# Kernel optimization log

Hardware: AMD Instinct MI355X
Metric: run time of the kernel (lower is better)

The kernel has to match this reference:

```python
import jax, jax.numpy as jnp
import numpy as np

B, N, D_IN = 8, 1369, 768
S, D, ITERS = 7, 256, 3
RES, SIGMA = 37, 5.0
EPS = 1e-8


def _ln(x, g, b):
    m = jnp.mean(x, -1, keepdims=True)
    v = jnp.mean((x - m) ** 2, -1, keepdims=True)
    return (x - m) * jax.lax.rsqrt(v + 1e-5) * g + b


def _abs_grid():
    xs = jnp.linspace(-1.0, 1.0, RES)
    ys = jnp.linspace(-1.0, 1.0, RES)
    gx, gy = jnp.meshgrid(xs, ys, indexing='xy')
    return jnp.stack([gx.reshape(-1), gy.reshape(-1)], axis=-1)  # [N,2]


def setup_inputs() -> dict:
    key = jax.random.key(0)
    ks = jax.random.split(key, 40)
    i = iter(range(40))
    def w(shape, scale=0.02):
        return (jax.random.normal(ks[next(i)], shape, jnp.float32) * scale).astype(jnp.float32)
    def zeros(shape):
        return jnp.zeros(shape, jnp.float32)
    xav = float(np.sqrt(6.0 / (S + D)))
    inp = {
        'inputs': jax.random.normal(ks[next(i)], (B, N, D_IN), jnp.float32),
        'slots_init_p': jax.random.uniform(ks[next(i)], (1, S, D), jnp.float32, -xav, xav),
        'S_s0': w((1, S, 1, 2)),
        'S_p0': w((1, S, 1, 2)),
        'im_ln1_g': jnp.ones((D_IN,), jnp.float32), 'im_ln1_b': zeros((D_IN,)),
        'im_w1': w((D_IN, D_IN)), 'im_b1': zeros((D_IN,)),
        'im_w2': w((D_IN, D)), 'im_b2': zeros((D,)),
        'im_ln2_g': jnp.ones((D,), jnp.float32), 'im_ln2_b': zeros((D,)),
        'Wq': w((D, D)), 'Wk': w((D, D)), 'Wv': w((D, D)),
        'g_w': w((2, D)), 'g_b': zeros((D,)),
        'f_w1': w((D, D)), 'f_b1': zeros((D,)),
        'f_w2': w((D, D)), 'f_b2': zeros((D,)),
        'ln_g': jnp.ones((D,), jnp.float32), 'ln_b': zeros((D,)),
        'gru_wih': w((D, 3 * D)), 'gru_whh': w((D, 3 * D)),
        'gru_bih': zeros((3 * D,)), 'gru_bhh': zeros((3 * D,)),
        'mlp_ln_g': jnp.ones((D,), jnp.float32), 'mlp_ln_b': zeros((D,)),
        'mlp_w1': w((D, 4 * D)), 'mlp_b1': zeros((4 * D,)),
        'mlp_w2': w((4 * D, D)), 'mlp_b2': zeros((D,)),
        'fin_w': w((D, D)), 'fin_b': zeros((D,)),
    }
    return inp


def reference(inputs, slots_init_p, S_s0, S_p0,
              im_ln1_g, im_ln1_b, im_w1, im_b1, im_w2, im_b2, im_ln2_g, im_ln2_b,
              Wq, Wk, Wv, g_w, g_b, f_w1, f_b1, f_w2, f_b2,
              ln_g, ln_b, gru_wih, gru_whh, gru_bih, gru_bhh,
              mlp_ln_g, mlp_ln_b, mlp_w1, mlp_b1, mlp_w2, mlp_b2,
              fin_w, fin_b):
    abs_grid = _abs_grid()                    # [N,2], constant buffer
    ag = abs_grid[None, None]                 # [1,1,N,2]
    scale = D ** (-0.5)

    slots = jnp.broadcast_to(slots_init_p, (B, S, D))
    slots_init = slots

    # initial_mlp: LN -> Linear -> ReLU -> Linear -> LN (dropout-free eval path)
    x = _ln(inputs, im_ln1_g, im_ln1_b)
    x = jax.nn.relu(x @ im_w1 + im_b1)
    x = x @ im_w2 + im_b2
    x = _ln(x, im_ln2_g, im_ln2_b)            # [B,N,D]
    KX = x @ Wk                                # slot-independent part of K(inputs)
    VX = x @ Wv

    S_p = jnp.broadcast_to(S_p0, (B, S, 1, 2))
    S_s = jnp.broadcast_to(S_s0, (B, S, 1, 2))

    def f_mlp(z):
        return jax.nn.relu(z @ f_w1 + f_b1) @ f_w2 + f_b2

    attn = None
    slots_prev = slots
    for t in range(ITERS + 1):
        if t == ITERS - 1:  # query_opt straight-through trick
            slots = jax.lax.stop_gradient(slots) + slots_init - jax.lax.stop_gradient(slots_init)
        slots_prev = slots
        sn = _ln(slots, ln_g, ln_b)
        rel = (ag - S_p) / (S_s * SIGMA)      # [B,S,N,2]
        grel = rel @ g_w + g_b                # [B,S,N,D]
        k = f_mlp(KX[:, None] + grel)         # [B,S,N,D]
        v = f_mlp(VX[:, None] + grel)
        q = sn @ Wq                           # [B,S,D]
        dots = jnp.einsum('bsd,bsnd->bsn', q, k) * scale
        attn = jax.nn.softmax(dots, axis=1) + EPS   # softmax over slots
        attn = attn / jnp.sum(attn, -1, keepdims=True)
        updates = jnp.einsum('bsnd,bsn->bsd', v, attn)
        S_p = jnp.einsum('bsn,nd->bsd', attn, abs_grid)[:, :, None, :]
        S_s = jnp.sqrt(jnp.einsum('bsnd,bsn->bsd', (ag - S_p) ** 2, attn))[:, :, None, :]
        if t != ITERS:
            # GRUCell (torch gate order r,z,n)
            gi = updates @ gru_wih + gru_bih
            gh = slots_prev @ gru_whh + gru_bhh
            i_r, i_z, i_n = jnp.split(gi, 3, axis=-1)
            h_r, h_z, h_n = jnp.split(gh, 3, axis=-1)
            r = jax.nn.sigmoid(i_r + h_r)
            z = jax.nn.sigmoid(i_z + h_z)
            n = jnp.tanh(i_n + r * h_n)
            slots = (1.0 - z) * n + z * slots_prev
            # residual pre-norm MLP (dropout identity in eval)
            m = _ln(slots, mlp_ln_g, mlp_ln_b)
            m = jax.nn.relu(m @ mlp_w1 + mlp_b1) @ mlp_w2 + mlp_b2
            slots = slots + m
    out = slots_prev @ fin_w + fin_b
    return out, attn
```

## Files before the change

### kernel.cpp

```cpp
#include <hip/hip_runtime.h>

constexpr int CB   = 8;
constexpr int CN   = 1369;
constexpr int CDIN = 768;
constexpr int CS   = 7;
constexpr int CD   = 256;
constexpr int CITERS = 3;
constexpr int CRES = 37;
constexpr float CSIGMA = 5.0f;
constexpr int CBS = CB * CS;
constexpr int CBN = CB * CN;
constexpr int CKV = 2 * CD;
constexpr float LNEPS = 1e-5f;
constexpr float ATTN_EPS = 1e-8f;

typedef unsigned short u16;
typedef short bs8 __attribute__((ext_vector_type(8)));
typedef float f4 __attribute__((ext_vector_type(4)));

__device__ __forceinline__ float ag_x(int n) { return -1.f + (float)(n % CRES) * (2.f / 36.f); }
__device__ __forceinline__ float ag_y(int n) { return -1.f + (float)(n / CRES) * (2.f / 36.f); }

__device__ __forceinline__ u16 bf_rne(float f) {
    unsigned u = __float_as_uint(f);
    return (u16)((u + 0x7FFFu + ((u >> 16) & 1u)) >> 16);
}
__device__ __forceinline__ float bf_to_f(u16 h) { return __uint_as_float(((unsigned)h) << 16); }

__device__ __forceinline__ void split2b(float v, u16& h, u16& m) {
    h = bf_rne(v);
    m = bf_rne(v - bf_to_f(h));
}

__device__ __forceinline__ void async16(const u16* g, u16* l) {
    __builtin_amdgcn_global_load_lds(
        (const __attribute__((address_space(1))) unsigned int*)g,
        (__attribute__((address_space(3))) unsigned int*)l, 16, 0, 0);
}

__device__ __forceinline__ float block_reduce_sum(float v, float* sbuf) {
    #pragma unroll
    for (int off = 32; off > 0; off >>= 1) v += __shfl_down(v, off, 64);
    if ((threadIdx.x & 63) == 0) sbuf[threadIdx.x >> 6] = v;
    __syncthreads();
    if (threadIdx.x == 0) sbuf[0] = sbuf[0] + sbuf[1] + sbuf[2] + sbuf[3];
    __syncthreads();
    float r = sbuf[0];
    __syncthreads();
    return r;
}

__device__ __forceinline__ float block_reduce_sum128(float v, float* sbuf) {
    #pragma unroll
    for (int off = 32; off > 0; off >>= 1) v += __shfl_down(v, off, 64);
    if ((threadIdx.x & 63) == 0) sbuf[threadIdx.x >> 6] = v;
    __syncthreads();
    float r = sbuf[0] + sbuf[1];
    __syncthreads();
    return r;
}

__global__ __launch_bounds__(256) void ln_planes_kernel(const float* __restrict__ in,
        u16* __restrict__ Yh, u16* __restrict__ Ym,
        const float* __restrict__ g, const float* __restrict__ b, int d) {
    __shared__ float sbuf[8];
    int row = blockIdx.x, t = threadIdx.x;
    const float* x = in + (size_t)row * d;
    float v0 = x[t], v1 = 0.f, v2 = 0.f;
    if (d > 256) { v1 = x[t + 256]; v2 = x[t + 512]; }
    float mean = block_reduce_sum(v0 + v1 + v2, sbuf) / d;
    float d0 = v0 - mean, d1 = v1 - mean, d2 = v2 - mean;
    float pv = (d > 256) ? (d0 * d0 + d1 * d1 + d2 * d2) : (d0 * d0);
    float var = block_reduce_sum(pv, sbuf) / d;
    float rstd = rsqrtf(var + LNEPS);
    {
        float y = d0 * rstd * g[t] + b[t];
        u16 h, m; split2b(y, h, m);
        Yh[(size_t)row * d + t] = h; Ym[(size_t)row * d + t] = m;
    }
    if (d > 256) {
        float y1 = d1 * rstd * g[t + 256] + b[t + 256];
        u16 h, m; split2b(y1, h, m);
        Yh[(size_t)row * d + t + 256] = h; Ym[(size_t)row * d + t + 256] = m;
        float y2 = d2 * rstd * g[t + 512] + b[t + 512];
        split2b(y2, h, m);
        Yh[(size_t)row * d + t + 512] = h; Ym[(size_t)row * d + t + 512] = m;
    }
}

__global__ __launch_bounds__(256) void transpose_split2z_kernel(
        const float* __restrict__ W1, u16* __restrict__ T1h, u16* __restrict__ T1m,
        const float* __restrict__ W2, u16* __restrict__ T2h, u16* __restrict__ T2m) {
    __shared__ float tile[32][33];
    const float* W; u16 *Th, *Tm; int N;
    if (blockIdx.z == 0) { W = W1; Th = T1h; Tm = T1m; N = CDIN; }
    else                 { W = W2; Th = T2h; Tm = T2m; N = CD; if (blockIdx.x >= CD / 32) return; }
    int K = CDIN;
    int nb = blockIdx.x * 32, kb = blockIdx.y * 32;
    int tx = threadIdx.x & 31, ty = threadIdx.x >> 5;
    #pragma unroll
    for (int i = 0; i < 32; i += 8)
        tile[ty + i][tx] = W[(size_t)(kb + ty + i) * N + nb + tx];
    __syncthreads();
    #pragma unroll
    for (int i = 0; i < 32; i += 8) {
        float v = tile[tx][ty + i];
        u16 h, m; split2b(v, h, m);
        size_t idx = (size_t)(nb + ty + i) * K + kb + tx;
        Th[idx] = h; Tm[idx] = m;
    }
}

__global__ __launch_bounds__(256) void wprep_kernel(
        const float* __restrict__ Wk, const float* __restrict__ Wv,
        const float* __restrict__ Wq,
        const float* __restrict__ f_w1, const float* __restrict__ f_w2,
        u16* __restrict__ kvth, u16* __restrict__ kvtm, float* __restrict__ Pq,
        const float* __restrict__ wih, float* __restrict__ Pg,
        const float* __restrict__ g_w, const float* __restrict__ g_b,
        const float* __restrict__ f_b1,
        float* __restrict__ G2, float* __restrict__ gb1,
        const float* __restrict__ f_b2, const float* __restrict__ bih,
        float* __restrict__ bg, float* __restrict__ wqb) {
    __shared__ float arow[CD];
    int bid = blockIdx.x;
    int n = threadIdx.x;
    if (bid < 512) {
        const float* A = (bid < 256) ? Wk : Wv;
        int k = bid & 255;
        size_t poff = (bid < 256) ? 0 : (size_t)CD * CD;
        arow[n] = A[k * CD + n];
        __syncthreads();
        float acc = 0.f;
        for (int j = 0; j < CD; j++) acc += arow[j] * f_w1[(size_t)j * CD + n];
        u16 h, m; split2b(acc, h, m);
        kvth[poff + (size_t)n * CD + k] = h;
        kvtm[poff + (size_t)n * CD + k] = m;
    } else if (bid < 768) {
        int k = bid - 512;
        arow[n] = Wq[k * CD + n];
        __syncthreads();
        float acc = 0.f;
        for (int c = 0; c < CD; c++) acc += arow[c] * f_w2[(size_t)n * CD + c];
        Pq[(size_t)k * CD + n] = acc;
    } else if (bid < 1536) {
        int bid2 = bid - 768;
        int k = bid2 & 255;
        int ny = bid2 >> 8;
        arow[n] = f_w2[k * CD + n];
        __syncthreads();
        int nn = ny * 256 + n;
        float acc = 0.f;
        for (int j = 0; j < CD; j++) acc += arow[j] * wih[(size_t)j * (3 * CD) + nn];
        Pg[(size_t)k * (3 * CD) + nn] = acc;
    } else if (bid == 1536) {
        float a0 = 0.f, a1 = 0.f, ab = 0.f;
        for (int j = 0; j < CD; j++) {
            float w = f_w1[j * CD + n];
            a0 += g_w[j] * w;
            a1 += g_w[CD + j] * w;
            ab += g_b[j] * w;
        }
        G2[n] = a0; G2[CD + n] = a1; gb1[n] = ab + f_b1[n];
    } else if (bid <= 1539) {
        int nn = (bid - 1537) * 256 + n;
        float s = bih[nn];
        for (int c = 0; c < CD; c++) s += f_b2[c] * wih[(size_t)c * (3 * CD) + nn];
        bg[nn] = s;
    } else {
        float s = 0.f;
        for (int c = 0; c < CD; c++) s += Wq[n * CD + c] * f_b2[c];
        wqb[n] = s;
    }
}

template<int BN, int NBUF>
__global__ __launch_bounds__(256)
void hgemm2(const u16* __restrict__ Ah, const u16* __restrict__ Am,
            const u16* __restrict__ Bh, const u16* __restrict__ Bm,
            int M, int N, int K, const float* __restrict__ bias, int relu,
            float* __restrict__ Cf, u16* __restrict__ Ch, u16* __restrict__ Cm) {
    constexpr int BP = BN * 32;
    constexpr int SB = 4096 + 2 * BP;
    constexpr int NI = 2 + 2 * (BN / 64);
    constexpr int NF = BN / 32;
    constexpr int PP = BN / 64;
    __shared__ u16 smem[NBUF][SB];
    const int tid = threadIdx.x;

    int bx = blockIdx.x, by = blockIdx.y;
    {
        int gx = gridDim.x;
        int nwg = gx * gridDim.y;
        if (!(nwg & 7)) {
            int bid = by * gx + bx;
            int cpx = nwg >> 3;
            int s = (bid & 7) * cpx + (bid >> 3);
            bx = s % gx; by = s / gx;
        }
    }
    const int m0 = by * 64, n0 = bx * BN;
    const int w = tid >> 6, lane = tid & 63;
    const int wm = w & 1, wn = w >> 1;
    const int l15 = lane & 15, l4 = lane >> 4;

    const u16* srcp[NI];
    int dsto[NI];
    #pragma unroll
    for (int i = 0; i < NI; i++) {
        const u16* bp; int row, r, c;
        if (i < 2) {
            int qq = tid;
            r = qq >> 2;
            c = (qq & 3) ^ ((r ^ (r >> 2)) & 3);
            bp = (i == 0) ? Ah : Am;
            row = m0 + r; row = row < M ? row : M - 1;
            dsto[i] = i * 2048 + w * 512;
        } else {
            int ii = i - 2;
            int plane = ii / PP;
            int sub = ii % PP;
            int qq = sub * 256 + tid;
            r = qq >> 2;
            c = (qq & 3) ^ ((r ^ (r >> 2)) & 3);
            bp = plane ? Bm : Bh;
            row = n0 + r;
            dsto[i] = 4096 + plane * BP + sub * 2048 + w * 512;
        }
        srcp[i] = bp + (size_t)row * K + c * 8;
    }

    f4 acc[2][NF];
    #pragma unroll
    for (int i = 0; i < 2; i++)
        #pragma unroll
        for (int j = 0; j < NF; j++) acc[i][j] = (f4){0.f, 0.f, 0.f, 0.f};

    const int cx8 = (l4 ^ (l15 & 3) ^ ((l15 >> 2) & 3)) * 8;

    const int ns = K / 32;
    #pragma unroll
    for (int d = 0; d < NBUF - 1; d++)
        #pragma unroll
        for (int i = 0; i < NI; i++) async16(srcp[i] + d * 32, &smem[d][dsto[i]]);

    u16* c0 = &smem[0][0];
    u16* c1 = &smem[NBUF > 1 ? 1 : 0][0];
    u16* c2 = &smem[NBUF - 1][0];

    for (int k = 0; k < ns; k++) {
        if constexpr (NBUF == 3) {
            if (k + 2 < ns) {
                #pragma unroll
                for (int i = 0; i < NI; i++) async16(srcp[i] + (k + 2) * 32, c2 + dsto[i]);
                if constexpr (BN == 64) asm volatile("s_waitcnt vmcnt(8)" ::: "memory");
                else                     asm volatile("s_waitcnt vmcnt(12)" ::: "memory");
            } else if (k + 1 < ns) {
                if constexpr (BN == 64) asm volatile("s_waitcnt vmcnt(4)" ::: "memory");
                else                     asm volatile("s_waitcnt vmcnt(6)" ::: "memory");
            } else {
                asm volatile("s_waitcnt vmcnt(0)" ::: "memory");
            }
        } else {
            if (k + 1 < ns) {
                #pragma unroll
                for (int i = 0; i < NI; i++) async16(srcp[i] + (k + 1) * 32, c1 + dsto[i]);
                if constexpr (BN == 64) asm volatile("s_waitcnt vmcnt(4)" ::: "memory");
                else                     asm volatile("s_waitcnt vmcnt(6)" ::: "memory");
            } else {
                asm volatile("s_waitcnt vmcnt(0)" ::: "memory");
            }
        }
        __builtin_amdgcn_s_barrier();
        bs8 ah[2], am[2], bh[NF], bm[NF];
        #pragma unroll
        for (int f = 0; f < 2; f++) {
            int oa = (wm * 32 + f * 16 + l15) * 32 + cx8;
            ah[f] = *(const bs8*)(c0 + oa);
            am[f] = *(const bs8*)(c0 + 2048 + oa);
        }
        #pragma unroll
        for (int f = 0; f < NF; f++) {
            int ob = (wn * (NF * 16) + f * 16 + l15) * 32 + cx8;
            bh[f] = *(const bs8*)(c0 + 4096 + ob);
            bm[f] = *(const bs8*)(c0 + 4096 + BP + ob);
        }
        #pragma unroll
        for (int mf = 0; mf < 2; mf++)
            #pragma unroll
            for (int nf = 0; nf < NF; nf++) {
                acc[mf][nf] = __builtin_amdgcn_mfma_f32_16x16x32_bf16(am[mf], bh[nf], acc[mf][nf], 0, 0, 0);
                acc[mf][nf] = __builtin_amdgcn_mfma_f32_16x16x32_bf16(ah[mf], bm[nf], acc[mf][nf], 0, 0, 0);
                acc[mf][nf] = __builtin_amdgcn_mfma_f32_16x16x32_bf16(ah[mf], bh[nf], acc[mf][nf], 0, 0, 0);
            }
        asm volatile("" ::: "memory");
        __builtin_amdgcn_s_barrier();
        if constexpr (NBUF == 3) { u16* t_ = c0; c0 = c1; c1 = c2; c2 = t_; }
        else                     { u16* t_ = c0; c0 = c1; c1 = t_; }
    }

    #pragma unroll
    for (int mf = 0; mf < 2; mf++)
        #pragma unroll
        for (int i = 0; i < 4; i++) {
            int grow = m0 + wm * 32 + mf * 16 + l4 * 4 + i;
            if (grow < M) {
                #pragma unroll
                for (int nf = 0; nf < NF; nf++) {
                    int col = n0 + wn * (NF * 16) + nf * 16 + l15;
                    float v = acc[mf][nf][i] + (bias ? bias[col] : 0.f);
                    if (relu) v = fmaxf(v, 0.f);
                    if (Cf) Cf[(size_t)grow * N + col] = v;
                    else {
                        u16 h, m; split2b(v, h, m);
                        Ch[(size_t)grow * N + col] = h;
                        Cm[(size_t)grow * N + col] = m;
                    }
                }
            }
        }
}

__global__ __launch_bounds__(128) void rowgemm_kernel(const float* __restrict__ A,
        const float* __restrict__ W, const float* __restrict__ bias,
        float* __restrict__ C, int N, int K, int relu,
        const float* __restrict__ resid, const float* __restrict__ resb) {
    __shared__ float sA[1024];
    int r = blockIdx.x;
    int c = blockIdx.y * 128 + threadIdx.x;
    for (int i = threadIdx.x; i < K; i += 128) sA[i] = A[(size_t)r * K + i];
    __syncthreads();
    float a0 = 0.f, a1 = 0.f, a2 = 0.f, a3 = 0.f;
    #pragma unroll 4
    for (int k = 0; k < K; k += 4) {
        a0 += sA[k]     * W[(size_t)k * N + c];
        a1 += sA[k + 1] * W[(size_t)(k + 1) * N + c];
        a2 += sA[k + 2] * W[(size_t)(k + 2) * N + c];
        a3 += sA[k + 3] * W[(size_t)(k + 3) * N + c];
    }
    float v = (a0 + a1) + (a2 + a3) + (bias ? bias[c] : 0.f);
    if (relu) v = fmaxf(v, 0.f);
    if (resid) v += resid[(size_t)r * N + c] + resb[c];
    C[(size_t)r * N + c] = v;
}

__global__ __launch_bounds__(128) void rowgemmG_kernel(
        const float* __restrict__ A0, const float* __restrict__ W0,
        const float* __restrict__ b0, float* __restrict__ C0,
        const float* __restrict__ A1, const float* __restrict__ W1,
        const float* __restrict__ b1, float* __restrict__ C1,
        const float* __restrict__ msum, int N, int K) {
    __shared__ float sA[256];
    const float* A = blockIdx.z ? A1 : A0;
    const float* W = blockIdx.z ? W1 : W0;
    const float* B = blockIdx.z ? b1 : b0;
    float* C = blockIdx.z ? C1 : C0;
    int r = blockIdx.x;
    int c = blockIdx.y * 128 + threadIdx.x;
    float scl = blockIdx.z ? 1.f : 1.f / msum[r * 8];
    for (int i = threadIdx.x; i < K; i += 128) sA[i] = A[(size_t)r * K + i] * scl;
    __syncthreads();
    float a0 = 0.f, a1 = 0.f, a2 = 0.f, a3 = 0.f;
    #pragma unroll 4
    for (int k = 0; k < K; k += 4) {
        a0 += sA[k]     * W[(size_t)k * N + c];
        a1 += sA[k + 1] * W[(size_t)(k + 1) * N + c];
        a2 += sA[k + 2] * W[(size_t)(k + 2) * N + c];
        a3 += sA[k + 3] * W[(size_t)(k + 3) * N + c];
    }
    C[(size_t)r * N + c] = (a0 + a1) + (a2 + a3) + B[c];
}

__global__ __launch_bounds__(256) void init_kernel(const float* __restrict__ slots_init_p,
        const float* __restrict__ S_s0, const float* __restrict__ S_p0,
        float* __restrict__ slots, float* __restrict__ S_s, float* __restrict__ S_p) {
    int bs = blockIdx.x, t = threadIdx.x;
    int s = bs % CS;
    slots[bs * CD + t] = slots_init_p[s * CD + t];
    if (t < 2) { S_s[bs * 2 + t] = S_s0[s * 2 + t]; S_p[bs * 2 + t] = S_p0[s * 2 + t]; }
}

__global__ __launch_bounds__(256) void ln_slots_q_kernel(const float* __restrict__ slots,
        const float* __restrict__ ln_g, const float* __restrict__ ln_b,
        const float* __restrict__ wqb, const float* __restrict__ Pq,
        float* __restrict__ qwb, float* __restrict__ qb0) {
    __shared__ float sbuf[8];
    __shared__ float sN[CD];
    int row = blockIdx.x, t = threadIdx.x;
    float x = slots[row * CD + t];
    float mean = block_reduce_sum(x, sbuf) / CD;
    float d0 = x - mean;
    float var = block_reduce_sum(d0 * d0, sbuf) / CD;
    float sn = d0 * rsqrtf(var + LNEPS) * ln_g[t] + ln_b[t];
    sN[t] = sn;
    float qb = block_reduce_sum(sn * wqb[t], sbuf);
    if (t == 0) qb0[row] = qb;
    __syncthreads();
    float acc = 0.f;
    #pragma unroll 4
    for (int k = 0; k < CD; k++) acc += sN[k] * Pq[(size_t)k * CD + t];
    qwb[row * CD + t] = acc;
}

__global__ __launch_bounds__(256) void slotsup_kernel(const float* __restrict__ h1b,
        const float* __restrict__ w2, const float* __restrict__ b2,
        const float* __restrict__ snewb,
        const float* __restrict__ ln_g, const float* __restrict__ ln_b,
        const float* __restrict__ wqb, const float* __restrict__ Pq,
        float* __restrict__ slots, float* __restrict__ qwb, float* __restrict__ qb0) {
    __shared__ float sbuf[8];
    __shared__ float sH[4 * CD];
    __shared__ float sN[CD];
    int row = blockIdx.x, t = threadIdx.x;
    for (int i = t; i < 4 * CD; i += 256) sH[i] = h1b[(size_t)row * 4 * CD + i];
    __syncthreads();
    float a0 = 0.f, a1 = 0.f, a2 = 0.f, a3 = 0.f;
    #pragma unroll 4
    for (int k = 0; k < 4 * CD; k += 4) {
        a0 += sH[k]     * w2[(size_t)k * CD + t];
        a1 += sH[k + 1] * w2[(size_t)(k + 1) * CD + t];
        a2 += sH[k + 2] * w2[(size_t)(k + 2) * CD + t];
        a3 += sH[k + 3] * w2[(size_t)(k + 3) * CD + t];
    }
    float v = (a0 + a1) + (a2 + a3) + 0.f;
    v += snewb[row * CD + t] + b2[t];
    slots[row * CD + t] = v;
    float mean = block_reduce_sum(v, sbuf) / CD;
    float d0 = v - mean;
    float var = block_reduce_sum(d0 * d0, sbuf) / CD;
    float sn = d0 * rsqrtf(var + LNEPS) * ln_g[t] + ln_b[t];
    sN[t] = sn;
    float qb = block_reduce_sum(sn * wqb[t], sbuf);
    if (t == 0) qb0[row] = qb;
    __syncthreads();
    float acc = 0.f;
    #pragma unroll 4
    for (int k = 0; k < CD; k++) acc += sN[k] * Pq[(size_t)k * CD + t];
    qwb[row * CD + t] = acc;
}

__global__ __launch_bounds__(256) void dotsv_kernel(const float* __restrict__ KVX,
        const float* __restrict__ S_p, const float* __restrict__ S_s,
        const float* __restrict__ msum_in, int useMsum,
        const float* __restrict__ G2, const float* __restrict__ gb1,
        const float* __restrict__ qw, const float* __restrict__ qb0,
        float* __restrict__ attn, float* __restrict__ Wacc,
        float* __restrict__ msum_out) {
    __shared__ float sred[4 * CD];
    int b = blockIdx.x;
    int w = threadIdx.x >> 6, l = threadIdx.x & 63;
    int k4 = l * 4;
    float4 g0 = *(const float4*)(G2 + k4);
    float4 g1 = *(const float4*)(G2 + CD + k4);
    float4 gb = *(const float4*)(gb1 + k4);
    float4 qwv[CS]; float px[CS], py[CS], ix[CS], iy[CS], q0[CS];
    #pragma unroll
    for (int s = 0; s < CS; s++) {
        int bs = b * CS + s;
        qwv[s] = *(const float4*)(qw + bs * CD + k4);
        if (useMsum) {
            const float* mp = msum_in + bs * 8;
            float m0 = mp[0];
            float pxv = mp[1] / m0, pyv = mp[2] / m0;
            float sx = sqrtf(fmaxf(mp[3] / m0 - pxv * pxv, 0.f));
            float sy = sqrtf(fmaxf(mp[4] / m0 - pyv * pyv, 0.f));
            px[s] = pxv; py[s] = pyv;
            ix[s] = 1.f / (sx * CSIGMA); iy[s] = 1.f / (sy * CSIGMA);
        } else {
            px[s] = S_p[2 * bs]; py[s] = S_p[2 * bs + 1];
            ix[s] = 1.f / (S_s[2 * bs] * CSIGMA); iy[s] = 1.f / (S_s[2 * bs + 1] * CSIGMA);
        }
        q0[s] = qb0[bs];
    }
    float4 acc[CS];
    #pragma unroll
    for (int s = 0; s < CS; s++) acc[s] = make_float4(0.f, 0.f, 0.f, 0.f);
    float wmv = 0.f;
    int sidx = l / 5;
    int jidx = l - sidx * 5;
    int nbase = blockIdx.y * 16 + w * 4;
    #pragma unroll
    for (int i = 0; i < 4; i++) {
        int n = nbase + i;
        int nc = n < CN ? n : CN - 1;
        const float* rowp = KVX + (size_t)(b * CN + nc) * CKV;
        float4 kx = *(const float4*)(rowp + k4);
        float ax = ag_x(nc), ay = ag_y(nc);
        float dsv[CS];
        #pragma unroll
        for (int s = 0; s < CS; s++) {
            float r0 = (ax - px[s]) * ix[s];
            float r1 = (ay - py[s]) * iy[s];
            float v0 = fmaxf(kx.x + r0 * g0.x + r1 * g1.x + gb.x, 0.f);
            float v1 = fmaxf(kx.y + r0 * g0.y + r1 * g1.y + gb.y, 0.f);
            float v2 = fmaxf(kx.z + r0 * g0.z + r1 * g1.z + gb.z, 0.f);
            float v3 = fmaxf(kx.w + r0 * g0.w + r1 * g1.w + gb.w, 0.f);
            float d = v0 * qwv[s].x + v1 * qwv[s].y + v2 * qwv[s].z + v3 * qwv[s].w;
            #pragma unroll
            for (int off = 32; off > 0; off >>= 1) d += __shfl_xor(d, off, 64);
            dsv[s] = 0.0625f * (d + q0[s]);
        }
        float mx = -1e30f;
        #pragma unroll
        for (int s = 0; s < CS; s++) mx = fmaxf(mx, dsv[s]);
        float sum = 0.f;
        #pragma unroll
        for (int s = 0; s < CS; s++) { dsv[s] = __expf(dsv[s] - mx); sum += dsv[s]; }
        float inv = 1.f / sum;
        #pragma unroll
        for (int s = 0; s < CS; s++) dsv[s] = dsv[s] * inv + ATTN_EPS;
        if (attn && l == 0 && n < CN) {
            #pragma unroll
            for (int s = 0; s < CS; s++)
                attn[(size_t)(b * CS + s) * CN + n] = dsv[s];
        }
        if (msum_out && n < CN) {
            float ax2 = ax * ax, ay2 = ay * ay;
            float a = dsv[0];
            a = (sidx == 1) ? dsv[1] : a;
            a = (sidx == 2) ? dsv[2] : a;
            a = (sidx == 3) ? dsv[3] : a;
            a = (sidx == 4) ? dsv[4] : a;
            a = (sidx == 5) ? dsv[5] : a;
            a = (sidx == 6) ? dsv[6] : a;
            float coef = 1.f;
            coef = (jidx == 1) ? ax : coef;
            coef = (jidx == 2) ? ay : coef;
            coef = (jidx == 3) ? ax2 : coef;
            coef = (jidx == 4) ? ay2 : coef;
            wmv += a * coef;
        }
        if (Wacc && n < CN) {
            float4 vx = *(const float4*)(rowp + CD + k4);
            #pragma unroll
            for (int s = 0; s < CS; s++) {
                float r0 = (ax - px[s]) * ix[s];
                float r1 = (ay - py[s]) * iy[s];
                float a = dsv[s];
                acc[s].x += a * fmaxf(vx.x + r0 * g0.x + r1 * g1.x + gb.x, 0.f);
                acc[s].y += a * fmaxf(vx.y + r0 * g0.y + r1 * g1.y + gb.y, 0.f);
                acc[s].z += a * fmaxf(vx.z + r0 * g0.z + r1 * g1.z + gb.z, 0.f);
                acc[s].w += a * fmaxf(vx.w + r0 * g0.w + r1 * g1.w + gb.w, 0.f);
            }
        }
    }
    if (Wacc) {
        for (int s = 0; s < CS; s++) {
            ((float4*)sred)[w * 64 + l] = acc[s];
            __syncthreads();
            if (threadIdx.x < CD) {
                float v = sred[threadIdx.x] + sred[CD + threadIdx.x]
                        + sred[2 * CD + threadIdx.x] + sred[3 * CD + threadIdx.x];
                atomicAdd(&Wacc[(size_t)(b * CS + s) * CD + threadIdx.x], v);
            }
            __syncthreads();
        }
    }
    if (msum_out) {
        if (l < 35) sred[w * 35 + l] = wmv;
        __syncthreads();
        if (threadIdx.x < 35) {
            float v = sred[threadIdx.x] + sred[35 + threadIdx.x]
                    + sred[70 + threadIdx.x] + sred[105 + threadIdx.x];
            int s = threadIdx.x / 5, j = threadIdx.x % 5;
            atomicAdd(&msum_out[(size_t)(b * CS + s) * 8 + j], v);
        }
    }
}

__global__ __launch_bounds__(256) void attn_scale_kernel(float* __restrict__ u,
        const float* __restrict__ msum) {
    int bs = blockIdx.x;
    float inv = 1.f / msum[(size_t)bs * 8];
    float* up = u + (size_t)bs * CN;
    for (int n = threadIdx.x; n < CN; n += 256) up[n] *= inv;
}

__global__ __launch_bounds__(128) void gate_mlp1_kernel(const float* __restrict__ giRaw,
        const float* __restrict__ ghRaw, const float* __restrict__ slots,
        const float* __restrict__ mg, const float* __restrict__ mb,
        const float* __restrict__ mlp_w1, const float* __restrict__ mlp_b1,
        float* __restrict__ snewb, float* __restrict__ h1b,
        float* __restrict__ WaccZ, float* __restrict__ msumZ) {
    __shared__ float sbuf[4];
    __shared__ float sM[CD];
    int row = blockIdx.x, t = threadIdx.x;
    float snew[2];
    #pragma unroll
    for (int e = 0; e < 2; e++) {
        int tt = t + e * 128;
        float gi0 = giRaw[row * 3 * CD + tt];
        float gi1 = giRaw[row * 3 * CD + CD + tt];
        float gi2 = giRaw[row * 3 * CD + 2 * CD + tt];
        float gh0 = ghRaw[row * 3 * CD + tt];
        float gh1 = ghRaw[row * 3 * CD + CD + tt];
        float gh2 = ghRaw[row * 3 * CD + 2 * CD + tt];
        float r = 1.f / (1.f + expf(-(gi0 + gh0)));
        float z = 1.f / (1.f + expf(-(gi1 + gh1)));
        float nn = tanhf(gi2 + r * gh2);
        snew[e] = (1.f - z) * nn + z * slots[row * CD + tt];
    }
    if (blockIdx.y == 0) {
        snewb[row * CD + t] = snew[0];
        snewb[row * CD + t + 128] = snew[1];
        WaccZ[row * CD + t] = 0.f;
        WaccZ[row * CD + t + 128] = 0.f;
        if (t < 8) msumZ[row * 8 + t] = 0.f;
    }
    float mean = block_reduce_sum128(snew[0] + snew[1], sbuf) / CD;
    float d0 = snew[0] - mean, d1 = snew[1] - mean;
    float var = block_reduce_sum128(d0 * d0 + d1 * d1, sbuf) / CD;
    float rstd = rsqrtf(var + LNEPS);
    sM[t]       = d0 * rstd * mg[t] + mb[t];
    sM[t + 128] = d1 * rstd * mg[t + 128] + mb[t + 128];
    __syncthreads();
    int c = blockIdx.y * 128 + t;
    float a0 = 0.f, a1 = 0.f, a2 = 0.f, a3 = 0.f;
    #pragma unroll 4
    for (int k = 0; k < CD; k += 4) {
        a0 += sM[k]     * mlp_w1[(size_t)k * (4 * CD) + c];
        a1 += sM[k + 1] * mlp_w1[(size_t)(k + 1) * (4 * CD) + c];
        a2 += sM[k + 2] * mlp_w1[(size_t)(k + 2) * (4 * CD) + c];
        a3 += sM[k + 3] * mlp_w1[(size_t)(k + 3) * (4 * CD) + c];
    }
    h1b[(size_t)row * (4 * CD) + c] = fmaxf((a0 + a1) + (a2 + a3) + mlp_b1[c], 0.f);
}

extern "C" void kernel_launch(void* const* d_in, const int* in_sizes, int n_in,
                              void* d_out, int out_size, void* d_ws, size_t ws_size,
                              hipStream_t stream) {
    (void)in_sizes; (void)n_in; (void)out_size;
    const float* inputs       = (const float*)d_in[0];
    const float* slots_init_p = (const float*)d_in[1];
    const float* S_s0         = (const float*)d_in[2];
    const float* S_p0         = (const float*)d_in[3];
    const float* im_ln1_g = (const float*)d_in[4];
    const float* im_ln1_b = (const float*)d_in[5];
    const float* im_w1    = (const float*)d_in[6];
    const float* im_b1    = (const float*)d_in[7];
    const float* im_w2    = (const float*)d_in[8];
    const float* im_b2    = (const float*)d_in[9];
    const float* im_ln2_g = (const float*)d_in[10];
    const float* im_ln2_b = (const float*)d_in[11];
    const float* Wq  = (const float*)d_in[12];
    const float* Wk  = (const float*)d_in[13];
    const float* Wv  = (const float*)d_in[14];
    const float* g_w = (const float*)d_in[15];
    const float* g_b = (const float*)d_in[16];
    const float* f_w1 = (const float*)d_in[17];
    const float* f_b1 = (const float*)d_in[18];
    const float* f_w2 = (const float*)d_in[19];
    const float* f_b2 = (const float*)d_in[20];
    const float* ln_g = (const float*)d_in[21];
    const float* ln_b = (const float*)d_in[22];
    const float* gru_wih = (const float*)d_in[23];
    const float* gru_whh = (const float*)d_in[24];
    const float* gru_bih = (const float*)d_in[25];
    const float* gru_bhh = (const float*)d_in[26];
    const float* mlp_ln_g = (const float*)d_in[27];
    const float* mlp_ln_b = (const float*)d_in[28];
    const float* mlp_w1 = (const float*)d_in[29];
    const float* mlp_b1 = (const float*)d_in[30];
    const float* mlp_w2 = (const float*)d_in[31];
    const float* mlp_b2 = (const float*)d_in[32];
    const float* fin_w = (const float*)d_in[33];
    const float* fin_b = (const float*)d_in[34];

    char* base = (char*)d_ws;
    size_t off = 0;
    auto take = [&](size_t bytes) { void* p = base + off; off += (bytes + 255) & ~(size_t)255; return p; };

    float* R1 = (float*)take((size_t)CBN * CDIN * 4);
    float* R2 = (float*)take((size_t)CBN * CDIN * 4);
    u16* w1th = (u16*)take((size_t)CDIN * CDIN * 2);
    u16* w1tm = (u16*)take((size_t)CDIN * CDIN * 2);
    u16* w2th = (u16*)take((size_t)CDIN * CD * 2);
    u16* w2tm = (u16*)take((size_t)CDIN * CD * 2);
    u16* kvth = (u16*)take((size_t)CKV * CD * 2);
    u16* kvtm = (u16*)take((size_t)CKV * CD * 2);
    float* G2b  = (float*)take((size_t)2 * CD * 4);
    float* gb1b = (float*)take((size_t)CD * 4);
    float* Pq   = (float*)take((size_t)CD * CD * 4);
    float* Pg   = (float*)take((size_t)CD * 3 * CD * 4);
    float* bgv  = (float*)take((size_t)3 * CD * 4);
    float* wqbb = (float*)take((size_t)CD * 4);
    float* qwb   = (float*)take((size_t)CBS * CD * 4);
    float* qb0b  = (float*)take((size_t)CBS * 4);
    float* Wacc  = (float*)take(((size_t)CBS * CD + 2 * CBS * 8) * 4);
    float* msumA = Wacc + (size_t)CBS * CD;
    float* msumB = msumA + (size_t)CBS * 8;
    float* giRaw = (float*)take((size_t)CBS * 3 * CD * 4);
    float* ghRaw = (float*)take((size_t)CBS * 3 * CD * 4);
    float* snewb = (float*)take((size_t)CBS * CD * 4);
    float* h1b   = (float*)take((size_t)CBS * 4 * CD * 4);
    float* S_pB  = (float*)take((size_t)CBS * 2 * 4);
    float* S_sB  = (float*)take((size_t)CBS * 2 * 4);
    float* slots = (float*)take((size_t)CBS * CD * 4);
    if (ws_size < off) return;

    float* msum[2] = {msumA, msumB};

    u16* xlnh = (u16*)R1;
    u16* xlnm = xlnh + (size_t)CBN * CDIN;
    u16* X1h  = (u16*)R2;
    u16* X1m  = X1h + (size_t)CBN * CDIN;
    float* xD = R1;
    u16* xDnh = (u16*)(R1 + (size_t)CBN * CD);
    u16* xDnm = xDnh + (size_t)CBN * CD;
    float* KVX = R2;

    float* out0 = (float*)d_out;
    float* attnb = out0 + CBS * CD;

    dim3 blk(256);
    const int gM = (CBN + 63) / 64;
    dim3 gridBN(CB, 86);

    transpose_split2z_kernel<<<dim3(CDIN/32, CDIN/32, 2), blk, 0, stream>>>(
        im_w1, w1th, w1tm, im_w2, w2th, w2tm);
    wprep_kernel<<<dim3(1541), blk, 0, stream>>>(Wk, Wv, Wq, f_w1, f_w2,
        kvth, kvtm, Pq, gru_wih, Pg, g_w, g_b, f_b1, G2b, gb1b,
        f_b2, gru_bih, bgv, wqbb);
    hipMemsetAsync(Wacc, 0, ((size_t)CBS * CD + 2 * CBS * 8) * sizeof(float), stream);

    ln_planes_kernel<<<CBN, blk, 0, stream>>>(inputs, xlnh, xlnm, im_ln1_g, im_ln1_b, CDIN);
    hgemm2<128,2><<<dim3(CDIN/128, gM), blk, 0, stream>>>(xlnh, xlnm, w1th, w1tm,
        CBN, CDIN, CDIN, im_b1, 1, nullptr, X1h, X1m);
    hgemm2<64,3><<<dim3(CD/64, gM), blk, 0, stream>>>(X1h, X1m, w2th, w2tm,
        CBN, CD, CDIN, im_b2, 0, xD, nullptr, nullptr);
    ln_planes_kernel<<<CBN, blk, 0, stream>>>(xD, xDnh, xDnm, im_ln2_g, im_ln2_b, CD);
    hgemm2<64,3><<<dim3(CKV/64, gM), blk, 0, stream>>>(xDnh, xDnm, kvth, kvtm,
        CBN, CKV, CD, nullptr, 0, KVX, nullptr, nullptr);
    init_kernel<<<CBS, blk, 0, stream>>>(slots_init_p, S_s0, S_p0, slots, S_sB, S_pB);

    ln_slots_q_kernel<<<CBS, blk, 0, stream>>>(slots, ln_g, ln_b, wqbb, Pq, qwb, qb0b);

    for (int t = 0; t < CITERS; t++) {
        dotsv_kernel<<<gridBN, blk, 0, stream>>>(KVX, S_pB, S_sB,
            msum[(t + 1) & 1], t > 0 ? 1 : 0, G2b, gb1b,
            qwb, qb0b, nullptr, Wacc, msum[t & 1]);
        rowgemmG_kernel<<<dim3(CBS, 3*CD/128, 2), dim3(128), 0, stream>>>(
            Wacc, Pg, bgv, giRaw, slots, gru_whh, gru_bhh, ghRaw, msum[t & 1], 3 * CD, CD);
        gate_mlp1_kernel<<<dim3(CBS, 8), dim3(128), 0, stream>>>(giRaw, ghRaw, slots,
            mlp_ln_g, mlp_ln_b, mlp_w1, mlp_b1, snewb, h1b, Wacc, msum[(t + 1) & 1]);
        slotsup_kernel<<<CBS, blk, 0, stream>>>(h1b, mlp_w2, mlp_b2, snewb,
            ln_g, ln_b, wqbb, Pq, slots, qwb, qb0b);
    }
    dotsv_kernel<<<gridBN, blk, 0, stream>>>(KVX, S_pB, S_sB,
        msum[0], 1, G2b, gb1b, qwb, qb0b, attnb, nullptr, msum[1]);
    attn_scale_kernel<<<CBS, blk, 0, stream>>>(attnb, msum[1]);

    rowgemm_kernel<<<dim3(CBS, CD/128), dim3(128), 0, stream>>>(slots, fin_w, fin_b,
        out0, CD, CD, 0, nullptr, nullptr);
}
```

Before: 613.8 us.

## Fuse MLP second layer into gate kernel via atomics and merge small launches

Moves the MLP w2 product into gate_mlp1_kernel: each block computes its 128-wide slice of the hidden layer, multiplies it by the matching rows of w2, and atomically accumulates into a slots accumulator. slotsup then reads and zeroes that accumulator instead of doing the full 1024-deep matvec. The init and slot-LN/q kernels are merged into one, and the attention rescale is merged with the final projection into a single launch. This is meant to cut kernel launches and the h1b round trip through global memory. In exchange it adds atomic contention and makes the floating-point summation order nondeterministic.

```diff
diff --git a/kernel.cpp b/kernel.cpp
--- a/kernel.cpp
+++ b/kernel.cpp
@@ -321,29 +321,6 @@
         }
 }
 
-__global__ __launch_bounds__(128) void rowgemm_kernel(const float* __restrict__ A,
-        const float* __restrict__ W, const float* __restrict__ bias,
-        float* __restrict__ C, int N, int K, int relu,
-        const float* __restrict__ resid, const float* __restrict__ resb) {
-    __shared__ float sA[1024];
-    int r = blockIdx.x;
-    int c = blockIdx.y * 128 + threadIdx.x;
-    for (int i = threadIdx.x; i < K; i += 128) sA[i] = A[(size_t)r * K + i];
-    __syncthreads();
-    float a0 = 0.f, a1 = 0.f, a2 = 0.f, a3 = 0.f;
-    #pragma unroll 4
-    for (int k = 0; k < K; k += 4) {
-        a0 += sA[k]     * W[(size_t)k * N + c];
-        a1 += sA[k + 1] * W[(size_t)(k + 1) * N + c];
-        a2 += sA[k + 2] * W[(size_t)(k + 2) * N + c];
-        a3 += sA[k + 3] * W[(size_t)(k + 3) * N + c];
-    }
-    float v = (a0 + a1) + (a2 + a3) + (bias ? bias[c] : 0.f);
-    if (relu) v = fmaxf(v, 0.f);
-    if (resid) v += resid[(size_t)r * N + c] + resb[c];
-    C[(size_t)r * N + c] = v;
-}
-
 __global__ __launch_bounds__(128) void rowgemmG_kernel(
         const float* __restrict__ A0, const float* __restrict__ W0,
         const float* __restrict__ b0, float* __restrict__ C0,
@@ -371,23 +348,19 @@
     C[(size_t)r * N + c] = (a0 + a1) + (a2 + a3) + B[c];
 }
 
-__global__ __launch_bounds__(256) void init_kernel(const float* __restrict__ slots_init_p,
+__global__ __launch_bounds__(256) void init_ln_q_kernel(const float* __restrict__ slots_init_p,
         const float* __restrict__ S_s0, const float* __restrict__ S_p0,
-        float* __restrict__ slots, float* __restrict__ S_s, float* __restrict__ S_p) {
-    int bs = blockIdx.x, t = threadIdx.x;
-    int s = bs % CS;
-    slots[bs * CD + t] = slots_init_p[s * CD + t];
-    if (t < 2) { S_s[bs * 2 + t] = S_s0[s * 2 + t]; S_p[bs * 2 + t] = S_p0[s * 2 + t]; }
-}
-
-__global__ __launch_bounds__(256) void ln_slots_q_kernel(const float* __restrict__ slots,
         const float* __restrict__ ln_g, const float* __restrict__ ln_b,
         const float* __restrict__ wqb, const float* __restrict__ Pq,
+        float* __restrict__ slots, float* __restrict__ S_s, float* __restrict__ S_p,
         float* __restrict__ qwb, float* __restrict__ qb0) {
     __shared__ float sbuf[8];
     __shared__ float sN[CD];
     int row = blockIdx.x, t = threadIdx.x;
-    float x = slots[row * CD + t];
+    int s = row % CS;
+    float x = slots_init_p[s * CD + t];
+    slots[row * CD + t] = x;
+    if (t < 2) { S_s[row * 2 + t] = S_s0[s * 2 + t]; S_p[row * 2 + t] = S_p0[s * 2 + t]; }
     float mean = block_reduce_sum(x, sbuf) / CD;
     float d0 = x - mean;
     float var = block_reduce_sum(d0 * d0, sbuf) / CD;
@@ -402,28 +375,16 @@
     qwb[row * CD + t] = acc;
 }
 
-__global__ __launch_bounds__(256) void slotsup_kernel(const float* __restrict__ h1b,
-        const float* __restrict__ w2, const float* __restrict__ b2,
-        const float* __restrict__ snewb,
+__global__ __launch_bounds__(256) void slotsup_kernel(float* __restrict__ slotsAcc,
+        const float* __restrict__ b2, const float* __restrict__ snewb,
         const float* __restrict__ ln_g, const float* __restrict__ ln_b,
         const float* __restrict__ wqb, const float* __restrict__ Pq,
         float* __restrict__ slots, float* __restrict__ qwb, float* __restrict__ qb0) {
     __shared__ float sbuf[8];
-    __shared__ float sH[4 * CD];
     __shared__ float sN[CD];
     int row = blockIdx.x, t = threadIdx.x;
-    for (int i = t; i < 4 * CD; i += 256) sH[i] = h1b[(size_t)row * 4 * CD + i];
-    __syncthreads();
-    float a0 = 0.f, a1 = 0.f, a2 = 0.f, a3 = 0.f;
-    #pragma unroll 4
-    for (int k = 0; k < 4 * CD; k += 4) {
-        a0 += sH[k]     * w2[(size_t)k * CD + t];
-        a1 += sH[k + 1] * w2[(size_t)(k + 1) * CD + t];
-        a2 += sH[k + 2] * w2[(size_t)(k + 2) * CD + t];
-        a3 += sH[k + 3] * w2[(size_t)(k + 3) * CD + t];
-    }
-    float v = (a0 + a1) + (a2 + a3) + 0.f;
-    v += snewb[row * CD + t] + b2[t];
+    float v = snewb[row * CD + t] + b2[t] + slotsAcc[row * CD + t];
+    slotsAcc[row * CD + t] = 0.f;
     slots[row * CD + t] = v;
     float mean = block_reduce_sum(v, sbuf) / CD;
     float d0 = v - mean;
@@ -568,22 +529,16 @@
     }
 }
 
-__global__ __launch_bounds__(256) void attn_scale_kernel(float* __restrict__ u,
-        const float* __restrict__ msum) {
-    int bs = blockIdx.x;
-    float inv = 1.f / msum[(size_t)bs * 8];
-    float* up = u + (size_t)bs * CN;
-    for (int n = threadIdx.x; n < CN; n += 256) up[n] *= inv;
-}
-
 __global__ __launch_bounds__(128) void gate_mlp1_kernel(const float* __restrict__ giRaw,
         const float* __restrict__ ghRaw, const float* __restrict__ slots,
         const float* __restrict__ mg, const float* __restrict__ mb,
         const float* __restrict__ mlp_w1, const float* __restrict__ mlp_b1,
-        float* __restrict__ snewb, float* __restrict__ h1b,
+        const float* __restrict__ w2,
+        float* __restrict__ snewb, float* __restrict__ slotsAcc,
         float* __restrict__ WaccZ, float* __restrict__ msumZ) {
     __shared__ float sbuf[4];
     __shared__ float sM[CD];
+    __shared__ float sH1[128];
     int row = blockIdx.x, t = threadIdx.x;
     float snew[2];
     #pragma unroll
@@ -623,7 +578,44 @@
         a2 += sM[k + 2] * mlp_w1[(size_t)(k + 2) * (4 * CD) + c];
         a3 += sM[k + 3] * mlp_w1[(size_t)(k + 3) * (4 * CD) + c];
     }
-    h1b[(size_t)row * (4 * CD) + c] = fmaxf((a0 + a1) + (a2 + a3) + mlp_b1[c], 0.f);
+    sH1[t] = fmaxf((a0 + a1) + (a2 + a3) + mlp_b1[c], 0.f);
+    __syncthreads();
+    float p0 = 0.f, p1 = 0.f;
+    const float* w2b = w2 + (size_t)blockIdx.y * 128 * CD;
+    #pragma unroll 4
+    for (int cc = 0; cc < 128; cc++) {
+        float h = sH1[cc];
+        p0 += h * w2b[(size_t)cc * CD + t];
+        p1 += h * w2b[(size_t)cc * CD + t + 128];
+    }
+    atomicAdd(&slotsAcc[row * CD + t], p0);
+    atomicAdd(&slotsAcc[row * CD + t + 128], p1);
+}
+
+__global__ __launch_bounds__(128) void final_kernel(const float* __restrict__ slots,
+        const float* __restrict__ fin_w, const float* __restrict__ fin_b,
+        float* __restrict__ out0, float* __restrict__ attn,
+        const float* __restrict__ msum) {
+    int row = blockIdx.x;
+    if (blockIdx.y == 2) {
+        float inv = 1.f / msum[(size_t)row * 8];
+        float* up = attn + (size_t)row * CN;
+        for (int n = threadIdx.x; n < CN; n += 128) up[n] *= inv;
+        return;
+    }
+    __shared__ float sA[CD];
+    for (int i = threadIdx.x; i < CD; i += 128) sA[i] = slots[(size_t)row * CD + i];
+    __syncthreads();
+    int c = blockIdx.y * 128 + threadIdx.x;
+    float a0 = 0.f, a1 = 0.f, a2 = 0.f, a3 = 0.f;
+    #pragma unroll 4
+    for (int k = 0; k < CD; k += 4) {
+        a0 += sA[k]     * fin_w[(size_t)k * CD + c];
+        a1 += sA[k + 1] * fin_w[(size_t)(k + 1) * CD + c];
+        a2 += sA[k + 2] * fin_w[(size_t)(k + 2) * CD + c];
+        a3 += sA[k + 3] * fin_w[(size_t)(k + 3) * CD + c];
+    }
+    out0[(size_t)row * CD + c] = (a0 + a1) + (a2 + a3) + fin_b[c];
 }
 
 extern "C" void kernel_launch(void* const* d_in, const int* in_sizes, int n_in,
@@ -686,13 +678,13 @@
     float* wqbb = (float*)take((size_t)CD * 4);
     float* qwb   = (float*)take((size_t)CBS * CD * 4);
     float* qb0b  = (float*)take((size_t)CBS * 4);
-    float* Wacc  = (float*)take(((size_t)CBS * CD + 2 * CBS * 8) * 4);
+    float* Wacc  = (float*)take(((size_t)CBS * CD * 2 + 2 * CBS * 8) * 4);
     float* msumA = Wacc + (size_t)CBS * CD;
     float* msumB = msumA + (size_t)CBS * 8;
+    float* slotsAcc = msumB + (size_t)CBS * 8;
     float* giRaw = (float*)take((size_t)CBS * 3 * CD * 4);
     float* ghRaw = (float*)take((size_t)CBS * 3 * CD * 4);
     float* snewb = (float*)take((size_t)CBS * CD * 4);
-    float* h1b   = (float*)take((size_t)CBS * 4 * CD * 4);
     float* S_pB  = (float*)take((size_t)CBS * 2 * 4);
     float* S_sB  = (float*)take((size_t)CBS * 2 * 4);
     float* slots = (float*)take((size_t)CBS * CD * 4);
@@ -721,7 +713,7 @@
     wprep_kernel<<<dim3(1541), blk, 0, stream>>>(Wk, Wv, Wq, f_w1, f_w2,
         kvth, kvtm, Pq, gru_wih, Pg, g_w, g_b, f_b1, G2b, gb1b,
         f_b2, gru_bih, bgv, wqbb);
-    hipMemsetAsync(Wacc, 0, ((size_t)CBS * CD + 2 * CBS * 8) * sizeof(float), stream);
+    hipMemsetAsync(Wacc, 0, ((size_t)CBS * CD * 2 + 2 * CBS * 8) * sizeof(float), stream);
 
     ln_planes_kernel<<<CBN, blk, 0, stream>>>(inputs, xlnh, xlnm, im_ln1_g, im_ln1_b, CDIN);
     hgemm2<128,2><<<dim3(CDIN/128, gM), blk, 0, stream>>>(xlnh, xlnm, w1th, w1tm,
@@ -731,9 +723,8 @@
     ln_planes_kernel<<<CBN, blk, 0, stream>>>(xD, xDnh, xDnm, im_ln2_g, im_ln2_b, CD);
     hgemm2<64,3><<<dim3(CKV/64, gM), blk, 0, stream>>>(xDnh, xDnm, kvth, kvtm,
         CBN, CKV, CD, nullptr, 0, KVX, nullptr, nullptr);
-    init_kernel<<<CBS, blk, 0, stream>>>(slots_init_p, S_s0, S_p0, slots, S_sB, S_pB);
-
-    ln_slots_q_kernel<<<CBS, blk, 0, stream>>>(slots, ln_g, ln_b, wqbb, Pq, qwb, qb0b);
+    init_ln_q_kernel<<<CBS, blk, 0, stream>>>(slots_init_p, S_s0, S_p0,
+        ln_g, ln_b, wqbb, Pq, slots, S_sB, S_pB, qwb, qb0b);
 
     for (int t = 0; t < CITERS; t++) {
         dotsv_kernel<<<gridBN, blk, 0, stream>>>(KVX, S_pB, S_sB,
@@ -742,14 +733,13 @@
         rowgemmG_kernel<<<dim3(CBS, 3*CD/128, 2), dim3(128), 0, stream>>>(
             Wacc, Pg, bgv, giRaw, slots, gru_whh, gru_bhh, ghRaw, msum[t & 1], 3 * CD, CD);
         gate_mlp1_kernel<<<dim3(CBS, 8), dim3(128), 0, stream>>>(giRaw, ghRaw, slots,
-            mlp_ln_g, mlp_ln_b, mlp_w1, mlp_b1, snewb, h1b, Wacc, msum[(t + 1) & 1]);
-        slotsup_kernel<<<CBS, blk, 0, stream>>>(h1b, mlp_w2, mlp_b2, snewb,
+            mlp_ln_g, mlp_ln_b, mlp_w1, mlp_b1, mlp_w2, snewb, slotsAcc,
+            Wacc, msum[(t + 1) & 1]);
+        slotsup_kernel<<<CBS, blk, 0, stream>>>(slotsAcc, mlp_b2, snewb,
             ln_g, ln_b, wqbb, Pq, slots, qwb, qb0b);
     }
     dotsv_kernel<<<gridBN, blk, 0, stream>>>(KVX, S_pB, S_sB,
         msum[0], 1, G2b, gb1b, qwb, qb0b, attnb, nullptr, msum[1]);
-    attn_scale_kernel<<<CBS, blk, 0, stream>>>(attnb, msum[1]);
-
-    rowgemm_kernel<<<dim3(CBS, CD/128), dim3(128), 0, stream>>>(slots, fin_w, fin_b,
-        out0, CD, CD, 0, nullptr, nullptr);
-}
+    final_kernel<<<dim3(CBS, 3), dim3(128), 0, stream>>>(slots, fin_w, fin_b,
+        out0, attnb, msum[1]);
+}
```

After: 561.7 us. 1.09x faster.
